# Optimization experiments

Hardware: AMD Instinct MI355X
Metric: run time of the kernel (lower is better)

Reference implementation:

```python
import jax, jax.numpy as jnp
import numpy as np

LN_EPS = 1e-5  # torch LayerNorm default
ITERS = 3

def _ln(x, g, b):
    m = jnp.mean(x, -1, keepdims=True)
    v = jnp.var(x, -1, keepdims=True)
    return (x - m) * jax.lax.rsqrt(v + LN_EPS) * g + b

def setup_inputs() -> dict:
    key = jax.random.key(0)
    ks = jax.random.split(key, 10)
    B, N, D, S, H = 32, 4096, 256, 8, 512
    sc = D ** -0.5
    w = lambda k, shape, s: jax.random.normal(k, shape, jnp.float32) * s
    return {
        "inputs": w(ks[0], (B, N, D), 1.0),
        "noise": w(ks[1], (B, S, D), 1.0),
        "ln_in_g": jnp.ones((D,), jnp.float32), "ln_in_b": jnp.zeros((D,), jnp.float32),
        "ln_slot_g": jnp.ones((D,), jnp.float32), "ln_slot_b": jnp.zeros((D,), jnp.float32),
        "ln_mlp_g": jnp.ones((D,), jnp.float32), "ln_mlp_b": jnp.zeros((D,), jnp.float32),
        "slot_mu": jnp.zeros((1, 1, D), jnp.float32),
        "slot_sigma": jnp.ones((1, 1, D), jnp.float32),
        "Wq": w(ks[2], (D, D), sc), "Wk": w(ks[3], (D, D), sc), "Wv": w(ks[4], (D, D), sc),
        "W_ih": w(ks[5], (D, 3 * D), sc), "W_hh": w(ks[6], (D, 3 * D), sc),
        "b_ih": jnp.zeros((3 * D,), jnp.float32), "b_hh": jnp.zeros((3 * D,), jnp.float32),
        "W1": w(ks[7], (D, H), sc), "b1": jnp.zeros((H,), jnp.float32),
        "W2": w(ks[8], (H, D), H ** -0.5), "b2": jnp.zeros((D,), jnp.float32),
    }

def reference(inputs, noise, ln_in_g, ln_in_b, ln_slot_g, ln_slot_b, ln_mlp_g, ln_mlp_b,
              slot_mu, slot_sigma, Wq, Wk, Wv, W_ih, W_hh, b_ih, b_hh, W1, b1, W2, b2):
    b, n, d = inputs.shape
    scale = d ** -0.5
    x = _ln(inputs, ln_in_g, ln_in_b)
    sigma = jnp.clip(jax.nn.softplus(slot_sigma), 0.1, 2.0)
    slots = slot_mu + sigma * noise            # [b, S, d]
    k = x @ Wk                                  # [b, n, d]
    v = x @ Wv                                  # [b, n, d]
    for _ in range(ITERS):
        slots_prev = slots
        s = _ln(slots, ln_slot_g, ln_slot_b)
        q = s @ Wq                              # [b, S, d]
        dots = jnp.einsum('bnd,bsd->bns', k, q) * scale
        attn = jax.nn.softmax(dots, axis=1)     # softmax over inputs (dim=1), as in source
        updates = jnp.einsum('bns,bnd->bsd', attn, v)
        # torch GRUCell: gate order (reset, update, new)
        gx = updates @ W_ih + b_ih
        gh = slots_prev @ W_hh + b_hh
        xr, xz, xn = jnp.split(gx, 3, -1)
        hr, hz, hn = jnp.split(gh, 3, -1)
        r = jax.nn.sigmoid(xr + hr)
        z = jax.nn.sigmoid(xz + hz)
        ng = jnp.tanh(xn + r * hn)
        slots = (1.0 - z) * ng + z * slots_prev
        m = _ln(slots, ln_mlp_g, ln_mlp_b)
        slots = slots + (jax.nn.relu(m @ W1 + b1) @ W2 + b2)
    return slots
```

## Files before the change

### kernel.cpp

```cpp
#include <hip/hip_runtime.h>

typedef unsigned short u16;
typedef unsigned int u32;
typedef short bf16x8 __attribute__((ext_vector_type(8)));
typedef float f32x4 __attribute__((ext_vector_type(4)));

#define DEV static __device__ __forceinline__

constexpr float LN_EPS = 1e-5f;
constexpr float SCALE = 0.0625f;

DEV float bf2f(u32 u) { return __uint_as_float(u << 16); }
DEV float bfe(short x) { return __uint_as_float(((u32)(u16)x) << 16); }
DEV u16 f2bf(float f) {
  u32 u = __float_as_uint(f);
  return (u16)((u + 0x7fffu + ((u >> 16) & 1u)) >> 16);
}
DEV u32 pk2(float a, float b) { return (u32)f2bf(a) | ((u32)f2bf(b) << 16); }


__global__ __launch_bounds__(256) void k_convert(
    const float* __restrict__ Wk, const float* __restrict__ Wv,
    const float* __restrict__ Wih, const float* __restrict__ Whh,
    const float* __restrict__ W1, const float* __restrict__ W2,
    const float* __restrict__ Wq,
    u16* __restrict__ wkvT, u16* __restrict__ wih_f, u16* __restrict__ whh_f,
    u16* __restrict__ w1_f, u16* __restrict__ w2_f, u16* __restrict__ wq_f,
    u16* __restrict__ wqt) {
  int idx = blockIdx.x * 256 + threadIdx.x;
  if (idx < 131072) {
    int n = idx >> 8, k = idx & 255;
    float v = (n < 256) ? Wk[k * 256 + n] : Wv[k * 256 + (n - 256)];
    wkvT[idx] = f2bf(v);
    return;
  }
  idx -= 131072;
  if (idx < 196608) {
    int j = idx & 7, lane = (idx >> 3) & 63, tile = idx >> 9;
    int kt = tile & 7, nt = tile >> 3;
    int k = kt * 32 + ((lane >> 4) << 3) + j, n = nt * 16 + (lane & 15);
    wih_f[idx] = f2bf(Wih[k * 768 + n]);
    return;
  }
  idx -= 196608;
  if (idx < 196608) {
    int j = idx & 7, lane = (idx >> 3) & 63, tile = idx >> 9;
    int kt = tile & 7, nt = tile >> 3;
    int k = kt * 32 + ((lane >> 4) << 3) + j, n = nt * 16 + (lane & 15);
    whh_f[idx] = f2bf(Whh[k * 768 + n]);
    return;
  }
  idx -= 196608;
  if (idx < 131072) {
    int j = idx & 7, lane = (idx >> 3) & 63, tile = idx >> 9;
    int kt = tile & 7, nt = tile >> 3;
    int k = kt * 32 + ((lane >> 4) << 3) + j, n = nt * 16 + (lane & 15);
    w1_f[idx] = f2bf(W1[k * 512 + n]);
    return;
  }
  idx -= 131072;
  if (idx < 131072) {
    int j = idx & 7, lane = (idx >> 3) & 63, tile = idx >> 9;
    int kt = tile & 15, nt = tile >> 4;
    int k = kt * 32 + ((lane >> 4) << 3) + j, n = nt * 16 + (lane & 15);
    w2_f[idx] = f2bf(W2[k * 256 + n]);
    return;
  }
  idx -= 131072;
  if (idx < 65536) {
    int j = idx & 7, lane = (idx >> 3) & 63, tile = idx >> 9;
    int kt = tile & 7, nt = tile >> 3;
    int k = kt * 32 + ((lane >> 4) << 3) + j, n = nt * 16 + (lane & 15);
    wq_f[idx] = f2bf(Wq[k * 256 + n]);
    return;
  }
  idx -= 65536;
  if (idx < 65536) {
    int t = idx >> 8, d = idx & 255;
    wqt[idx] = f2bf(Wq[d * 256 + t]);
    return;
  }
}

__global__ __launch_bounds__(256) void k_ln(const float* __restrict__ in,
    const float* __restrict__ g, const float* __restrict__ b,
    u16* __restrict__ xbf) {
  int row = blockIdx.x * 4 + (threadIdx.x >> 6);
  int lane = threadIdx.x & 63;
  float4 v = ((const float4*)(in + (size_t)row * 256))[lane];
  float s = v.x + v.y + v.z + v.w;
  float ss = v.x * v.x + v.y * v.y + v.z * v.z + v.w * v.w;
#pragma unroll
  for (int o = 32; o; o >>= 1) { s += __shfl_xor(s, o); ss += __shfl_xor(ss, o); }
  float mean = s * (1.f / 256.f);
  float rstd = rsqrtf(ss * (1.f / 256.f) - mean * mean + LN_EPS);
  float4 gv = ((const float4*)g)[lane];
  float4 bv = ((const float4*)b)[lane];
  uint2 o;
  o.x = pk2((v.x - mean) * rstd * gv.x + bv.x, (v.y - mean) * rstd * gv.y + bv.y);
  o.y = pk2((v.z - mean) * rstd * gv.z + bv.z, (v.w - mean) * rstd * gv.w + bv.w);
  ((uint2*)(xbf + (size_t)row * 256))[lane] = o;
}

__global__ __launch_bounds__(256) void k_slots_init(
    const float* __restrict__ noise, const float* __restrict__ mu,
    const float* __restrict__ sig, const float* __restrict__ g,
    const float* __restrict__ b, const u16* __restrict__ wqt,
    float* __restrict__ slots, float* __restrict__ qbuf) {
  int bs = blockIdx.x, t = threadIdx.x;
  float sg = sig[t];
  float sp = (sg > 20.f) ? sg : log1pf(expf(sg));
  sp = fminf(fmaxf(sp, 0.1f), 2.0f);
  float sl = mu[t] + sp * noise[bs * 256 + t];
  slots[bs * 256 + t] = sl;
  __shared__ float red[8];
  __shared__ __align__(16) float sln[256];
  float s = sl, ss = sl * sl;
#pragma unroll
  for (int o = 32; o; o >>= 1) { s += __shfl_xor(s, o); ss += __shfl_xor(ss, o); }
  int w = t >> 6;
  if ((t & 63) == 0) { red[w] = s; red[4 + w] = ss; }
  __syncthreads();
  s = red[0] + red[1] + red[2] + red[3];
  ss = red[4] + red[5] + red[6] + red[7];
  float mean = s * (1.f / 256.f);
  float rstd = rsqrtf(ss * (1.f / 256.f) - mean * mean + LN_EPS);
  sln[t] = (sl - mean) * rstd * g[t] + b[t];
  __syncthreads();
  float acc = 0.f;
  const bf16x8* wqp = (const bf16x8*)(wqt + t * 256);
#pragma unroll 4
  for (int db = 0; db < 32; ++db) {
    float q8[8];
    *(float4*)q8 = *(const float4*)&sln[db * 8];
    *(float4*)(q8 + 4) = *(const float4*)&sln[db * 8 + 4];
    bf16x8 wv = wqp[db];
#pragma unroll
    for (int j = 0; j < 8; ++j) acc += q8[j] * bfe(wv[j]);
  }
  qbuf[bs * 256 + t] = acc;
}

__global__ __launch_bounds__(256) void k_gemm(
    const u16* __restrict__ X, const u16* __restrict__ Wt,
    u16* __restrict__ kT, u16* __restrict__ vT) {
  __shared__ u16 smem[16896];
  int bid = (blockIdx.x & 7) * 512 + (blockIdx.x >> 3);
  int mt = bid >> 2, nt = bid & 3;
  int w = threadIdx.x >> 6, lane = threadIdx.x & 63;
  int wr = w >> 1, wc = w & 1;
  f32x4 acc[4][4] = {};
  for (int ks = 0; ks < 4; ++ks) {
#pragma unroll
    for (int i = 0; i < 4; ++i) {
      int cbase = (w * 4 + i) * 64;
      int c = cbase + lane;
      int r = c >> 3;
      int swz = (c & 7) ^ (r & 7);
      const u16* srcA = X + (mt * 128 + r) * 256 + ks * 64 + swz * 8;
      const u16* srcB = Wt + (nt * 128 + r) * 256 + ks * 64 + swz * 8;
      __builtin_amdgcn_global_load_lds(
          (const __attribute__((address_space(1))) void*)srcA,
          (__attribute__((address_space(3))) void*)(smem + cbase * 8), 16, 0, 0);
      __builtin_amdgcn_global_load_lds(
          (const __attribute__((address_space(1))) void*)srcB,
          (__attribute__((address_space(3))) void*)(smem + 8192 + cbase * 8), 16, 0, 0);
    }
    __syncthreads();
#pragma unroll
    for (int kk = 0; kk < 2; ++kk) {
      bf16x8 af[4], bfr[4];
#pragma unroll
      for (int m = 0; m < 4; ++m) {
        int lrow = wr * 64 + m * 16 + (lane & 15);
        int slot = (kk * 4 + (lane >> 4)) ^ (lrow & 7);
        af[m] = *(const bf16x8*)((const char*)smem + lrow * 128 + slot * 16);
      }
#pragma unroll
      for (int n = 0; n < 4; ++n) {
        int lcol = wc * 64 + n * 16 + (lane & 15);
        int slot = (kk * 4 + (lane >> 4)) ^ (lcol & 7);
        bfr[n] = *(const bf16x8*)((const char*)smem + 16384 + lcol * 128 + slot * 16);
      }
#pragma unroll
      for (int m = 0; m < 4; ++m)
#pragma unroll
        for (int n = 0; n < 4; ++n)
          acc[m][n] = __builtin_amdgcn_mfma_f32_16x16x32_bf16(af[m], bfr[n], acc[m][n], 0, 0, 0);
    }
    __syncthreads();
  }
  int bb = (mt * 128) >> 12;
  int nb0 = (mt * 128) & 4095;
#pragma unroll
  for (int m = 0; m < 4; ++m)
#pragma unroll
    for (int n = 0; n < 4; ++n) {
      int col = wc * 64 + n * 16 + (lane & 15);
      int r0 = wr * 64 + m * 16 + (lane >> 4) * 4;
      uint2 pk;
      pk.x = pk2(acc[m][n][0], acc[m][n][1]);
      pk.y = pk2(acc[m][n][2], acc[m][n][3]);
      *(uint2*)((char*)smem + col * 264 + r0 * 2) = pk;
    }
  __syncthreads();
  u16* outp = (nt < 2 ? kT : vT) + (size_t)bb * (1 << 20) + (nt & 1) * 128 * 4096 + nb0;
  for (int i = 0; i < 32; ++i) {
    int dl = w * 32 + i;
    u32 val = *(const u32*)((const char*)smem + dl * 264 + lane * 4);
    *(u32*)(outp + dl * 4096 + 2 * lane) = val;
  }
}

__global__ __launch_bounds__(128) void k_dots(
    const u16* __restrict__ kT, const float* __restrict__ qbuf,
    float* __restrict__ pml, u16* __restrict__ plT) {
  int bid = (blockIdx.x & 7) * 64 + (blockIdx.x >> 3);
  int b = bid >> 4, c = bid & 15;
  int n0 = c * 256;
  int t = threadIdx.x, w = t >> 6, lane = t & 63;
  __shared__ __align__(16) float qT[256][8];
  __shared__ float red[16];
  for (int i = t; i < 2048; i += 128) {
    int s = i >> 8, d = i & 255;
    qT[d][s] = qbuf[(b * 8 + s) * 256 + d];
  }
  __syncthreads();
  float acc[8][2] = {};
  const u16* kp = kT + (size_t)b * (1 << 20) + n0 + 2 * t;
#pragma unroll 8
  for (int d = 0; d < 256; ++d) {
    u32 kk = *(const u32*)(kp + (size_t)d * 4096);
    float k0 = bf2f(kk & 0xffffu), k1 = bf2f(kk >> 16);
    float q8[8];
    *(float4*)q8 = *(const float4*)&qT[d][0];
    *(float4*)(q8 + 4) = *(const float4*)&qT[d][4];
#pragma unroll
    for (int s = 0; s < 8; ++s) { acc[s][0] += k0 * q8[s]; acc[s][1] += k1 * q8[s]; }
  }
  float mx[8];
#pragma unroll
  for (int s = 0; s < 8; ++s) {
    acc[s][0] *= SCALE; acc[s][1] *= SCALE;
    float lm = fmaxf(acc[s][0], acc[s][1]);
#pragma unroll
    for (int o = 32; o; o >>= 1) lm = fmaxf(lm, __shfl_xor(lm, o));
    if (lane == 0) red[w * 8 + s] = lm;
  }
  __syncthreads();
#pragma unroll
  for (int s = 0; s < 8; ++s) mx[s] = fmaxf(red[s], red[8 + s]);
  __syncthreads();
  float pv0[8], pv1[8];
#pragma unroll
  for (int s = 0; s < 8; ++s) {
    pv0[s] = __expf(acc[s][0] - mx[s]);
    pv1[s] = __expf(acc[s][1] - mx[s]);
    float l = pv0[s] + pv1[s];
#pragma unroll
    for (int o = 32; o; o >>= 1) l += __shfl_xor(l, o);
    if (lane == 0) red[w * 8 + s] = l;
  }
  __syncthreads();
  if (t < 8) {
    pml[(b * 16 + c) * 16 + t] = mx[t];
    pml[(b * 16 + c) * 16 + 8 + t] = red[t] + red[8 + t];
  }
  u16* pp = plT + (size_t)b * 65536 + n0 + 2 * t;
#pragma unroll
  for (int s = 0; s < 8; ++s) {
    *(u32*)(pp + s * 4096) = pk2(pv0[s], pv1[s]);
    *(u32*)(pp + (8 + s) * 4096) = 0u;
  }
}

__global__ __launch_bounds__(256) void k_pv(
    const u16* __restrict__ plT, const u16* __restrict__ vT,
    const float* __restrict__ pml, u16* __restrict__ ufrag) {
  int bid = (blockIdx.x & 7) * 64 + (blockIdx.x >> 3);
  int b = bid >> 4, nt = bid & 15;
  int w = threadIdx.x >> 6, lane = threadIdx.x & 63;
  int r0 = (lane >> 4) * 4;
  float wcv[4][4];
  const float* pb = pml + b * 256;
#pragma unroll
  for (int j = 0; j < 4; ++j) {
    int s = r0 + j;
    if (s < 8) {
      float M = -1e30f;
#pragma unroll
      for (int c = 0; c < 16; ++c) M = fmaxf(M, pb[c * 16 + s]);
      float L = 0.f;
#pragma unroll
      for (int c = 0; c < 16; ++c) L += pb[c * 16 + 8 + s] * __expf(pb[c * 16 + s] - M);
      float invL = 1.f / L;
#pragma unroll
      for (int cc = 0; cc < 4; ++cc)
        wcv[cc][j] = __expf(pb[(w * 4 + cc) * 16 + s] - M) * invL;
    } else {
#pragma unroll
      for (int cc = 0; cc < 4; ++cc) wcv[cc][j] = 0.f;
    }
  }
  const u16* pA = plT + (size_t)b * 65536 + (lane & 15) * 4096 + ((lane >> 4) << 3);
  const u16* pB = vT + (size_t)b * (1 << 20) + (size_t)(nt * 16 + (lane & 15)) * 4096 + ((lane >> 4) << 3);
  f32x4 tot = {};
#pragma unroll
  for (int cc = 0; cc < 4; ++cc) {
    f32x4 acc = {};
    int kbase = (w * 4 + cc) * 256;
#pragma unroll
    for (int q = 0; q < 8; ++q) {
      int n = kbase + q * 32;
      bf16x8 a = *(const bf16x8*)(pA + n);
      bf16x8 bb = *(const bf16x8*)(pB + n);
      acc = __builtin_amdgcn_mfma_f32_16x16x32_bf16(a, bb, acc, 0, 0, 0);
    }
#pragma unroll
    for (int j = 0; j < 4; ++j) tot[j] += wcv[cc][j] * acc[j];
  }
  __shared__ __align__(16) float red[4][64][4];
  *(float4*)&red[w][lane][0] = *(float4*)&tot;
  __syncthreads();
  if (w == 0 && r0 < 8) {
    float4 t0 = *(float4*)&red[0][lane][0];
    float4 t1 = *(float4*)&red[1][lane][0];
    float4 t2 = *(float4*)&red[2][lane][0];
    float4 t3 = *(float4*)&red[3][lane][0];
    float rr[4] = {t0.x + t1.x + t2.x + t3.x, t0.y + t1.y + t2.y + t3.y,
                   t0.z + t1.z + t2.z + t3.z, t0.w + t1.w + t2.w + t3.w};
    int d = nt * 16 + (lane & 15);
    int mt = b >> 1, kt = d >> 5;
    int laneBase = ((d >> 3) & 3) * 16;
#pragma unroll
    for (int j = 0; j < 4; ++j) {
      int row16 = (b & 1) * 8 + r0 + j;
      ufrag[((mt * 8 + kt) * 64 + laneBase + row16) * 8 + (d & 7)] = f2bf(rr[j]);
    }
  }
}

__global__ __launch_bounds__(256) void k_gru2(
    const u16* __restrict__ ufrag, const float* __restrict__ slots_in,
    const u16* __restrict__ wih_f, const u16* __restrict__ whh_f,
    const float* __restrict__ bih, const float* __restrict__ bhh,
    float* __restrict__ snew) {
  __shared__ __align__(16) u16 hfl[4096];
  int bid = blockIdx.x;
  int mt = bid >> 2;
  int t = threadIdx.x, w = t >> 6, lane = t & 63;
  {
    int r16 = t >> 4, cg = t & 15;
    int row = mt * 16 + r16;
    int kt = cg >> 1;
    int laneLo = (cg & 1) * 32 + r16;
    int laneHi = laneLo + 16;
    const float4* hp = (const float4*)(slots_in + (size_t)row * 256 + cg * 16);
    float4 h0 = hp[0], h1 = hp[1], h2 = hp[2], h3 = hp[3];
    uint4 pk;
    pk.x = pk2(h0.x, h0.y); pk.y = pk2(h0.z, h0.w);
    pk.z = pk2(h1.x, h1.y); pk.w = pk2(h1.z, h1.w);
    *(uint4*)(hfl + (kt * 64 + laneLo) * 8) = pk;
    pk.x = pk2(h2.x, h2.y); pk.y = pk2(h2.z, h2.w);
    pk.z = pk2(h3.x, h3.y); pk.w = pk2(h3.z, h3.w);
    *(uint4*)(hfl + (kt * 64 + laneHi) * 8) = pk;
  }
  __syncthreads();
  int g = (bid & 3) * 4 + w;
  const bf16x8* wih = (const bf16x8*)wih_f;
  const bf16x8* whh = (const bf16x8*)whh_f;
  f32x4 ar = {}, az = {}, an = {}, hr = {}, hz = {}, hn = {};
#pragma unroll
  for (int kt = 0; kt < 8; ++kt) {
    bf16x8 au = *(const bf16x8*)(ufrag + ((mt * 8 + kt) * 64 + lane) * 8);
    bf16x8 ah = *(const bf16x8*)(hfl + (kt * 64 + lane) * 8);
    ar = __builtin_amdgcn_mfma_f32_16x16x32_bf16(au, wih[(g * 8 + kt) * 64 + lane], ar, 0, 0, 0);
    az = __builtin_amdgcn_mfma_f32_16x16x32_bf16(au, wih[((16 + g) * 8 + kt) * 64 + lane], az, 0, 0, 0);
    an = __builtin_amdgcn_mfma_f32_16x16x32_bf16(au, wih[((32 + g) * 8 + kt) * 64 + lane], an, 0, 0, 0);
    hr = __builtin_amdgcn_mfma_f32_16x16x32_bf16(ah, whh[(g * 8 + kt) * 64 + lane], hr, 0, 0, 0);
    hz = __builtin_amdgcn_mfma_f32_16x16x32_bf16(ah, whh[((16 + g) * 8 + kt) * 64 + lane], hz, 0, 0, 0);
    hn = __builtin_amdgcn_mfma_f32_16x16x32_bf16(ah, whh[((32 + g) * 8 + kt) * 64 + lane], hn, 0, 0, 0);
  }
  int tc = g * 16 + (lane & 15);
  float cr = bih[tc], cz = bih[256 + tc], cn = bih[512 + tc];
  float dr = bhh[tc], dz = bhh[256 + tc], dn = bhh[512 + tc];
#pragma unroll
  for (int j = 0; j < 4; ++j) {
    int row = mt * 16 + (lane >> 4) * 4 + j;
    float r = 1.f / (1.f + __expf(-(ar[j] + cr + hr[j] + dr)));
    float z = 1.f / (1.f + __expf(-(az[j] + cz + hz[j] + dz)));
    float ng = tanhf(an[j] + cn + r * (hn[j] + dn));
    float h = slots_in[row * 256 + tc];
    snew[row * 256 + tc] = (1.f - z) * ng + z * h;
  }
}

__global__ __launch_bounds__(256) void k_mlp1ln(
    const float* __restrict__ sn, const float* __restrict__ gm,
    const float* __restrict__ bm, const u16* __restrict__ w1_f,
    const float* __restrict__ b1v, u16* __restrict__ h1frag) {
  __shared__ __align__(16) u16 afr[4096];
  int w = threadIdx.x >> 6, lane = threadIdx.x & 63;
  int mt = blockIdx.x >> 3;
  int d0 = lane * 4;
  float4 gvv = *(const float4*)(gm + d0);
  float4 bvv = *(const float4*)(bm + d0);
#pragma unroll
  for (int i = 0; i < 4; ++i) {
    int r16 = w * 4 + i;
    float4 v = *(const float4*)(sn + (mt * 16 + r16) * 256 + d0);
    float s = v.x + v.y + v.z + v.w;
    float ss = v.x * v.x + v.y * v.y + v.z * v.z + v.w * v.w;
#pragma unroll
    for (int o = 32; o; o >>= 1) { s += __shfl_xor(s, o); ss += __shfl_xor(ss, o); }
    float mean = s * (1.f / 256.f);
    float rstd = rsqrtf(ss * (1.f / 256.f) - mean * mean + LN_EPS);
    uint2 pk;
    pk.x = pk2((v.x - mean) * rstd * gvv.x + bvv.x, (v.y - mean) * rstd * gvv.y + bvv.y);
    pk.y = pk2((v.z - mean) * rstd * gvv.z + bvv.z, (v.w - mean) * rstd * gvv.w + bvv.w);
    int kt = lane >> 3;
    int laneA = ((lane >> 1) & 3) * 16 + r16;
    *(uint2*)(afr + (kt * 64 + laneA) * 8 + (lane & 1) * 4) = pk;
  }
  __syncthreads();
  int nt = (blockIdx.x & 7) * 4 + w;
  const bf16x8* bw = (const bf16x8*)w1_f;
  f32x4 acc = {};
#pragma unroll
  for (int kt = 0; kt < 8; ++kt)
    acc = __builtin_amdgcn_mfma_f32_16x16x32_bf16(
        *(const bf16x8*)(afr + (kt * 64 + lane) * 8),
        bw[(nt * 8 + kt) * 64 + lane], acc, 0, 0, 0);
  int col = nt * 16 + (lane & 15);
  float bbv = b1v[col];
  int kt2 = col >> 5, j2 = col & 7;
  int laneBase = ((col >> 3) & 3) * 16;
#pragma unroll
  for (int j = 0; j < 4; ++j) {
    int r = (lane >> 4) * 4 + j;
    float vv = fmaxf(acc[j] + bbv, 0.f);
    h1frag[((mt * 16 + kt2) * 64 + laneBase + r) * 8 + j2] = f2bf(vv);
  }
}

__global__ __launch_bounds__(256) void k_mlp2(
    const u16* __restrict__ h1frag, const u16* __restrict__ w2_f,
    const float* __restrict__ b2v, const float* __restrict__ snew,
    float* __restrict__ sout) {
  int w = threadIdx.x >> 6, lane = threadIdx.x & 63;
  int unit = blockIdx.x * 4 + w;
  int mt = unit >> 4, nt = unit & 15;
  const bf16x8* bw = (const bf16x8*)w2_f;
  f32x4 acc = {};
#pragma unroll
  for (int kt = 0; kt < 16; ++kt)
    acc = __builtin_amdgcn_mfma_f32_16x16x32_bf16(
        *(const bf16x8*)(h1frag + ((mt * 16 + kt) * 64 + lane) * 8),
        bw[(nt * 16 + kt) * 64 + lane], acc, 0, 0, 0);
  int col = nt * 16 + (lane & 15);
  float bbv = b2v[col];
#pragma unroll
  for (int j = 0; j < 4; ++j) {
    int row = mt * 16 + (lane >> 4) * 4 + j;
    sout[row * 256 + col] = acc[j] + bbv + snew[row * 256 + col];
  }
}

__global__ __launch_bounds__(256) void k_qln(
    const float* __restrict__ so, const float* __restrict__ gsv,
    const float* __restrict__ bsv, const u16* __restrict__ wq_f,
    float* __restrict__ qbuf) {
  __shared__ __align__(16) u16 afr[4096];
  int w = threadIdx.x >> 6, lane = threadIdx.x & 63;
  int mt = blockIdx.x >> 2;
  int d0 = lane * 4;
  float4 gvv = *(const float4*)(gsv + d0);
  float4 bvv = *(const float4*)(bsv + d0);
#pragma unroll
  for (int i = 0; i < 4; ++i) {
    int r16 = w * 4 + i;
    float4 v = *(const float4*)(so + (mt * 16 + r16) * 256 + d0);
    float s = v.x + v.y + v.z + v.w;
    float ss = v.x * v.x + v.y * v.y + v.z * v.z + v.w * v.w;
#pragma unroll
    for (int o = 32; o; o >>= 1) { s += __shfl_xor(s, o); ss += __shfl_xor(ss, o); }
    float mean = s * (1.f / 256.f);
    float rstd = rsqrtf(ss * (1.f / 256.f) - mean * mean + LN_EPS);
    uint2 pk;
    pk.x = pk2((v.x - mean) * rstd * gvv.x + bvv.x, (v.y - mean) * rstd * gvv.y + bvv.y);
    pk.y = pk2((v.z - mean) * rstd * gvv.z + bvv.z, (v.w - mean) * rstd * gvv.w + bvv.w);
    int kt = lane >> 3;
    int laneA = ((lane >> 1) & 3) * 16 + r16;
    *(uint2*)(afr + (kt * 64 + laneA) * 8 + (lane & 1) * 4) = pk;
  }
  __syncthreads();
  int nt = (blockIdx.x & 3) * 4 + w;
  const bf16x8* bw = (const bf16x8*)wq_f;
  f32x4 acc = {};
#pragma unroll
  for (int kt = 0; kt < 8; ++kt)
    acc = __builtin_amdgcn_mfma_f32_16x16x32_bf16(
        *(const bf16x8*)(afr + (kt * 64 + lane) * 8),
        bw[(nt * 8 + kt) * 64 + lane], acc, 0, 0, 0);
  int col = nt * 16 + (lane & 15);
#pragma unroll
  for (int j = 0; j < 4; ++j) {
    int row = mt * 16 + (lane >> 4) * 4 + j;
    qbuf[row * 256 + col] = acc[j];
  }
}

extern "C" void kernel_launch(void* const* d_in, const int* in_sizes, int n_in,
                              void* d_out, int out_size, void* d_ws, size_t ws_size,
                              hipStream_t stream) {
  (void)in_sizes; (void)n_in; (void)out_size; (void)ws_size;
  const float* inputs    = (const float*)d_in[0];
  const float* noise     = (const float*)d_in[1];
  const float* ln_in_g   = (const float*)d_in[2];
  const float* ln_in_b   = (const float*)d_in[3];
  const float* ln_slot_g = (const float*)d_in[4];
  const float* ln_slot_b = (const float*)d_in[5];
  const float* ln_mlp_g  = (const float*)d_in[6];
  const float* ln_mlp_b  = (const float*)d_in[7];
  const float* slot_mu   = (const float*)d_in[8];
  const float* slot_sig  = (const float*)d_in[9];
  const float* Wq        = (const float*)d_in[10];
  const float* Wk        = (const float*)d_in[11];
  const float* Wv        = (const float*)d_in[12];
  const float* W_ih      = (const float*)d_in[13];
  const float* W_hh      = (const float*)d_in[14];
  const float* b_ih      = (const float*)d_in[15];
  const float* b_hh      = (const float*)d_in[16];
  const float* W1        = (const float*)d_in[17];
  const float* b1        = (const float*)d_in[18];
  const float* W2        = (const float*)d_in[19];
  const float* b2        = (const float*)d_in[20];

  char* p = (char*)d_ws;
  auto take = [&](size_t bytes) { char* r = p; p += (bytes + 255) & ~(size_t)255; return r; };
  u16* xbf      = (u16*)take((size_t)131072 * 256 * 2);
  u16* kT       = (u16*)take((size_t)32 * 256 * 4096 * 2);
  u16* vT       = (u16*)take((size_t)32 * 256 * 4096 * 2);
  u16* plT      = (u16*)take((size_t)32 * 16 * 4096 * 2);
  u16* wkvT     = (u16*)take(131072 * 2);
  u16* wih_f    = (u16*)take(196608 * 2);
  u16* whh_f    = (u16*)take(196608 * 2);
  u16* w1_f     = (u16*)take(131072 * 2);
  u16* w2_f     = (u16*)take(131072 * 2);
  u16* wq_f     = (u16*)take(65536 * 2);
  u16* wqt      = (u16*)take(65536 * 2);
  u16* ufrag    = (u16*)take(65536 * 2);
  u16* h1frag   = (u16*)take(131072 * 2);
  float* snew   = (float*)take(65536 * 4);
  float* slotsA = (float*)take(256 * 256 * 4);
  float* slotsB = (float*)take(256 * 256 * 4);
  float* qbuf   = (float*)take(256 * 256 * 4);
  float* pml    = (float*)take(32 * 16 * 16 * 4);

  k_convert<<<3584, 256, 0, stream>>>(Wk, Wv, W_ih, W_hh, W1, W2, Wq,
                                      wkvT, wih_f, whh_f, w1_f, w2_f, wq_f, wqt);
  k_ln<<<32768, 256, 0, stream>>>(inputs, ln_in_g, ln_in_b, xbf);
  k_slots_init<<<256, 256, 0, stream>>>(noise, slot_mu, slot_sig, ln_slot_g, ln_slot_b, wqt, slotsA, qbuf);
  k_gemm<<<4096, 256, 0, stream>>>(xbf, wkvT, kT, vT);

  const float* scur = slotsA;
  for (int it = 0; it < 3; ++it) {
    k_dots<<<512, 128, 0, stream>>>(kT, qbuf, pml, plT);
    k_pv<<<512, 256, 0, stream>>>(plT, vT, pml, ufrag);
    k_gru2<<<64, 256, 0, stream>>>(ufrag, scur, wih_f, whh_f, b_ih, b_hh, snew);
    k_mlp1ln<<<128, 256, 0, stream>>>(snew, ln_mlp_g, ln_mlp_b, w1_f, b1, h1frag);
    float* sout = (it == 2) ? (float*)d_out : ((it == 0) ? slotsB : slotsA);
    k_mlp2<<<64, 256, 0, stream>>>(h1frag, w2_f, b2, snew, sout);
    if (it < 2) k_qln<<<64, 256, 0, stream>>>(sout, ln_slot_g, ln_slot_b, wq_f, qbuf);
    scur = sout;
  }
}
```

Baseline: 291.0 us.

## Fuse input LayerNorm into K/V projection GEMM, keeping A tile in LDS

Removes the separate LayerNorm kernel and its bf16 intermediate buffer. Each block now loads 64 fp32 input rows, computes LayerNorm in registers, writes the bf16 A tile into swizzled LDS, then loops over all four 128-column N tiles of the combined Wk/Wv weight, streaming B tiles through LDS. This avoids writing and re-reading the normalized activations from global memory and stops re-reading A once per N tile. In exchange the B tile is single-buffered with a barrier before every k-step, and the larger LDS footprint lowers occupancy.

```diff
diff --git a/kernel.cpp b/kernel.cpp
--- a/kernel.cpp
+++ b/kernel.cpp
@@ -17,7 +17,6 @@
   return (u16)((u + 0x7fffu + ((u >> 16) & 1u)) >> 16);
 }
 DEV u32 pk2(float a, float b) { return (u32)f2bf(a) | ((u32)f2bf(b) << 16); }
-
 
 __global__ __launch_bounds__(256) void k_convert(
     const float* __restrict__ Wk, const float* __restrict__ Wv,
@@ -82,26 +81,6 @@
   }
 }
 
-__global__ __launch_bounds__(256) void k_ln(const float* __restrict__ in,
-    const float* __restrict__ g, const float* __restrict__ b,
-    u16* __restrict__ xbf) {
-  int row = blockIdx.x * 4 + (threadIdx.x >> 6);
-  int lane = threadIdx.x & 63;
-  float4 v = ((const float4*)(in + (size_t)row * 256))[lane];
-  float s = v.x + v.y + v.z + v.w;
-  float ss = v.x * v.x + v.y * v.y + v.z * v.z + v.w * v.w;
-#pragma unroll
-  for (int o = 32; o; o >>= 1) { s += __shfl_xor(s, o); ss += __shfl_xor(ss, o); }
-  float mean = s * (1.f / 256.f);
-  float rstd = rsqrtf(ss * (1.f / 256.f) - mean * mean + LN_EPS);
-  float4 gv = ((const float4*)g)[lane];
-  float4 bv = ((const float4*)b)[lane];
-  uint2 o;
-  o.x = pk2((v.x - mean) * rstd * gv.x + bv.x, (v.y - mean) * rstd * gv.y + bv.y);
-  o.y = pk2((v.z - mean) * rstd * gv.z + bv.z, (v.w - mean) * rstd * gv.w + bv.w);
-  ((uint2*)(xbf + (size_t)row * 256))[lane] = o;
-}
-
 __global__ __launch_bounds__(256) void k_slots_init(
     const float* __restrict__ noise, const float* __restrict__ mu,
     const float* __restrict__ sig, const float* __restrict__ g,
@@ -141,74 +120,122 @@
   qbuf[bs * 256 + t] = acc;
 }
 
-__global__ __launch_bounds__(256) void k_gemm(
-    const u16* __restrict__ X, const u16* __restrict__ Wt,
+__global__ __launch_bounds__(256) void k_lngemm(
+    const float* __restrict__ inF, const float* __restrict__ lng,
+    const float* __restrict__ lnb, const u16* __restrict__ Wt,
     u16* __restrict__ kT, u16* __restrict__ vT) {
-  __shared__ u16 smem[16896];
-  int bid = (blockIdx.x & 7) * 512 + (blockIdx.x >> 3);
-  int mt = bid >> 2, nt = bid & 3;
-  int w = threadIdx.x >> 6, lane = threadIdx.x & 63;
-  int wr = w >> 1, wc = w & 1;
-  f32x4 acc[4][4] = {};
-  for (int ks = 0; ks < 4; ++ks) {
+  __shared__ __align__(16) u16 smem[33280];
+  int mt = (blockIdx.x & 7) * 256 + (blockIdx.x >> 3);
+  int grow = mt * 64;
+  int bb = grow >> 12, nb0 = grow & 4095;
+  int t = threadIdx.x, w = t >> 6, lane = t & 63;
+  u16* Bbase = smem + 16384;
+  char* bounce = (char*)smem + 49152;
+  float* redp = (float*)bounce;
+
+  {
 #pragma unroll
     for (int i = 0; i < 4; ++i) {
       int cbase = (w * 4 + i) * 64;
       int c = cbase + lane;
-      int r = c >> 3;
-      int swz = (c & 7) ^ (r & 7);
-      const u16* srcA = X + (mt * 128 + r) * 256 + ks * 64 + swz * 8;
-      const u16* srcB = Wt + (nt * 128 + r) * 256 + ks * 64 + swz * 8;
-      __builtin_amdgcn_global_load_lds(
-          (const __attribute__((address_space(1))) void*)srcA,
-          (__attribute__((address_space(3))) void*)(smem + cbase * 8), 16, 0, 0);
+      int r = c >> 3, sc = c & 7;
+      const u16* srcB = Wt + r * 256 + ((sc ^ (r & 7)) << 3);
       __builtin_amdgcn_global_load_lds(
           (const __attribute__((address_space(1))) void*)srcB,
-          (__attribute__((address_space(3))) void*)(smem + 8192 + cbase * 8), 16, 0, 0);
+          (__attribute__((address_space(3))) void*)(Bbase + cbase * 8), 16, 0, 0);
+    }
+  }
+  float4 vv[16];
+  {
+    int r = t >> 2, q = t & 3;
+    const float4* src = (const float4*)(inF + (size_t)(grow + r) * 256 + q * 64);
+    float s = 0.f, ss = 0.f;
+#pragma unroll
+    for (int i = 0; i < 16; ++i) {
+      vv[i] = src[i];
+      s += vv[i].x + vv[i].y + vv[i].z + vv[i].w;
+      ss += vv[i].x * vv[i].x + vv[i].y * vv[i].y + vv[i].z * vv[i].z + vv[i].w * vv[i].w;
+    }
+    redp[r * 8 + q] = s;
+    redp[r * 8 + 4 + q] = ss;
+  }
+  __syncthreads();
+  {
+    int r = t >> 2, q = t & 3;
+    float s = redp[r * 8] + redp[r * 8 + 1] + redp[r * 8 + 2] + redp[r * 8 + 3];
+    float ss = redp[r * 8 + 4] + redp[r * 8 + 5] + redp[r * 8 + 6] + redp[r * 8 + 7];
+    float mean = s * (1.f / 256.f);
+    float rstd = rsqrtf(ss * (1.f / 256.f) - mean * mean + LN_EPS);
+    const float4* gp = (const float4*)(lng + q * 64);
+    const float4* bp = (const float4*)(lnb + q * 64);
+#pragma unroll
+    for (int j = 0; j < 8; ++j) {
+      float4 a = vv[2 * j], bfl = vv[2 * j + 1];
+      float4 gv0 = gp[2 * j], gv1 = gp[2 * j + 1];
+      float4 bv0 = bp[2 * j], bv1 = bp[2 * j + 1];
+      uint4 pk;
+      pk.x = pk2((a.x - mean) * rstd * gv0.x + bv0.x, (a.y - mean) * rstd * gv0.y + bv0.y);
+      pk.y = pk2((a.z - mean) * rstd * gv0.z + bv0.z, (a.w - mean) * rstd * gv0.w + bv0.w);
+      pk.z = pk2((bfl.x - mean) * rstd * gv1.x + bv1.x, (bfl.y - mean) * rstd * gv1.y + bv1.y);
+      pk.w = pk2((bfl.z - mean) * rstd * gv1.z + bv1.z, (bfl.w - mean) * rstd * gv1.w + bv1.w);
+      int cc = q * 8 + j;
+      *(uint4*)((char*)smem + r * 512 + ((cc ^ (r & 7)) << 4)) = pk;
+    }
+  }
+  f32x4 acc[8] = {};
+  for (int nt = 0; nt < 4; ++nt) {
+    for (int ks = 0; ks < 4; ++ks) {
+      __syncthreads();
+#pragma unroll
+      for (int kk = 0; kk < 2; ++kk) {
+        int lrow = w * 16 + (lane & 15);
+        int cc = ks * 8 + kk * 4 + (lane >> 4);
+        bf16x8 af = *(const bf16x8*)((const char*)smem + lrow * 512 + ((cc ^ (lrow & 7)) << 4));
+#pragma unroll
+        for (int n = 0; n < 8; ++n) {
+          int lcol = n * 16 + (lane & 15);
+          int slot = (kk * 4 + (lane >> 4)) ^ (lcol & 7);
+          bf16x8 bfr = *(const bf16x8*)((const char*)smem + 32768 + lcol * 128 + slot * 16);
+          acc[n] = __builtin_amdgcn_mfma_f32_16x16x32_bf16(af, bfr, acc[n], 0, 0, 0);
+        }
+      }
+      __syncthreads();
+      int nks = ks + 1, nnt = nt;
+      if (nks == 4) { nks = 0; nnt = nt + 1; }
+      if (nnt < 4) {
+#pragma unroll
+        for (int i = 0; i < 4; ++i) {
+          int cbase = (w * 4 + i) * 64;
+          int c = cbase + lane;
+          int r = c >> 3, sc = c & 7;
+          const u16* srcB = Wt + (nnt * 128 + r) * 256 + nks * 64 + ((sc ^ (r & 7)) << 3);
+          __builtin_amdgcn_global_load_lds(
+              (const __attribute__((address_space(1))) void*)srcB,
+              (__attribute__((address_space(3))) void*)(Bbase + cbase * 8), 16, 0, 0);
+        }
+      }
+    }
+#pragma unroll
+    for (int n = 0; n < 8; ++n) {
+      int col = n * 16 + (lane & 15);
+      int r0 = w * 16 + (lane >> 4) * 4;
+      uint2 pk;
+      pk.x = pk2(acc[n][0], acc[n][1]);
+      pk.y = pk2(acc[n][2], acc[n][3]);
+      *(uint2*)(bounce + col * 136 + r0 * 2) = pk;
+      acc[n] = (f32x4){0.f, 0.f, 0.f, 0.f};
     }
     __syncthreads();
-#pragma unroll
-    for (int kk = 0; kk < 2; ++kk) {
-      bf16x8 af[4], bfr[4];
-#pragma unroll
-      for (int m = 0; m < 4; ++m) {
-        int lrow = wr * 64 + m * 16 + (lane & 15);
-        int slot = (kk * 4 + (lane >> 4)) ^ (lrow & 7);
-        af[m] = *(const bf16x8*)((const char*)smem + lrow * 128 + slot * 16);
+    {
+      u16* outp = (nt < 2 ? kT : vT) + (size_t)bb * (1 << 20) + (nt & 1) * 128 * 4096 + nb0;
+      int d = t >> 1, seg = t & 1;
+#pragma unroll
+      for (int i = 0; i < 16; ++i) {
+        u32 val = *(const u32*)(bounce + d * 136 + seg * 64 + i * 4);
+        *(u32*)(outp + (size_t)d * 4096 + seg * 32 + i * 2) = val;
       }
-#pragma unroll
-      for (int n = 0; n < 4; ++n) {
-        int lcol = wc * 64 + n * 16 + (lane & 15);
-        int slot = (kk * 4 + (lane >> 4)) ^ (lcol & 7);
-        bfr[n] = *(const bf16x8*)((const char*)smem + 16384 + lcol * 128 + slot * 16);
-      }
-#pragma unroll
-      for (int m = 0; m < 4; ++m)
-#pragma unroll
-        for (int n = 0; n < 4; ++n)
-          acc[m][n] = __builtin_amdgcn_mfma_f32_16x16x32_bf16(af[m], bfr[n], acc[m][n], 0, 0, 0);
     }
     __syncthreads();
-  }
-  int bb = (mt * 128) >> 12;
-  int nb0 = (mt * 128) & 4095;
-#pragma unroll
-  for (int m = 0; m < 4; ++m)
-#pragma unroll
-    for (int n = 0; n < 4; ++n) {
-      int col = wc * 64 + n * 16 + (lane & 15);
-      int r0 = wr * 64 + m * 16 + (lane >> 4) * 4;
-      uint2 pk;
-      pk.x = pk2(acc[m][n][0], acc[m][n][1]);
-      pk.y = pk2(acc[m][n][2], acc[m][n][3]);
-      *(uint2*)((char*)smem + col * 264 + r0 * 2) = pk;
-    }
-  __syncthreads();
-  u16* outp = (nt < 2 ? kT : vT) + (size_t)bb * (1 << 20) + (nt & 1) * 128 * 4096 + nb0;
-  for (int i = 0; i < 32; ++i) {
-    int dl = w * 32 + i;
-    u32 val = *(const u32*)((const char*)smem + dl * 264 + lane * 4);
-    *(u32*)(outp + dl * 4096 + 2 * lane) = val;
   }
 }
 
@@ -538,7 +565,6 @@
 
   char* p = (char*)d_ws;
   auto take = [&](size_t bytes) { char* r = p; p += (bytes + 255) & ~(size_t)255; return r; };
-  u16* xbf      = (u16*)take((size_t)131072 * 256 * 2);
   u16* kT       = (u16*)take((size_t)32 * 256 * 4096 * 2);
   u16* vT       = (u16*)take((size_t)32 * 256 * 4096 * 2);
   u16* plT      = (u16*)take((size_t)32 * 16 * 4096 * 2);
@@ -559,9 +585,8 @@
 
   k_convert<<<3584, 256, 0, stream>>>(Wk, Wv, W_ih, W_hh, W1, W2, Wq,
                                       wkvT, wih_f, whh_f, w1_f, w2_f, wq_f, wqt);
-  k_ln<<<32768, 256, 0, stream>>>(inputs, ln_in_g, ln_in_b, xbf);
   k_slots_init<<<256, 256, 0, stream>>>(noise, slot_mu, slot_sig, ln_slot_g, ln_slot_b, wqt, slotsA, qbuf);
-  k_gemm<<<4096, 256, 0, stream>>>(xbf, wkvT, kT, vT);
+  k_lngemm<<<2048, 256, 0, stream>>>(inputs, ln_in_g, ln_in_b, wkvT, kT, vT);
 
   const float* scur = slotsA;
   for (int it = 0; it < 3; ++it) {
```

Measured after the change: 325.1 us. 11.7% more time.
